# Kernel optimization log

Measured on AMD Instinct MI355X. Metric: run time of the kernel, lower is better.

## Reference

```python
import jax, jax.numpy as jnp
import numpy as np

N_NODES = 20000
T_STEPS = 8


def _layer_norm(x, g, b, eps=1e-5):
    mu = x.mean(-1, keepdims=True)
    var = ((x - mu) ** 2).mean(-1, keepdims=True)
    return (x - mu) * jax.lax.rsqrt(var + eps) * g + b


def _linear(x, W, b):
    # torch nn.Linear: x @ W.T + b, W is [out, in]
    return x @ W.T + b


def _gcn_conv(xw, norm, src, dst, b, n):
    # xw: pre-transformed features [N, H]; symmetric-normalized aggregation
    msg = xw[src] * norm[:, None]
    return jax.ops.segment_sum(msg, dst, num_segments=n) + b


def setup_inputs() -> dict:
    key = jax.random.key(0)
    ks = jax.random.split(key, 16)
    N, T, K, E, D, H, M = N_NODES, T_STEPS, 4000, 400000, 128, 128, 16
    s = 0.05
    return {
        "node_t": jax.random.randint(ks[0], (T, K), 0, N),
        "edge_index_t": jax.random.randint(ks[1], (T, 2, E), 0, N),
        "m": M,
        "emb": jax.random.normal(ks[2], (N, D), jnp.float32) * s,
        "convW1": jax.random.normal(ks[3], (H, D), jnp.float32) * s,
        "convb1": jnp.zeros((H,), jnp.float32),
        "convW2": jax.random.normal(ks[4], (H, H), jnp.float32) * s,
        "convb2": jnp.zeros((H,), jnp.float32),
        "tn_g": jnp.ones((H,), jnp.float32),
        "tn_b": jnp.zeros((H,), jnp.float32),
        "tok_w1": jax.random.normal(ks[5], (M, M), jnp.float32) * s,
        "tok_b1": jnp.zeros((M,), jnp.float32),
        "tok_w2": jax.random.normal(ks[6], (M, M), jnp.float32) * s,
        "tok_b2": jnp.zeros((M,), jnp.float32),
        "cn_g": jnp.ones((H,), jnp.float32),
        "cn_b": jnp.zeros((H,), jnp.float32),
        "ch_w1": jax.random.normal(ks[7], (H, H), jnp.float32) * s,
        "ch_b1": jnp.zeros((H,), jnp.float32),
        "ch_w2": jax.random.normal(ks[8], (H, H), jnp.float32) * s,
        "ch_b2": jnp.zeros((H,), jnp.float32),
    }


def reference(node_t, edge_index_t, m, emb, convW1, convb1, convW2, convb2,
              tn_g, tn_b, tok_w1, tok_b1, tok_w2, tok_b2,
              cn_g, cn_b, ch_w1, ch_b1, ch_w2, ch_b2):
    N = emb.shape[0]
    H = convW1.shape[0]
    gelu = lambda x: jax.nn.gelu(x, approximate=False)

    def mixer(x):  # x: [N, m, H]
        y = _layer_norm(x, tn_g, tn_b)
        y = jnp.swapaxes(y, 1, 2)                 # [N, H, m]
        y = _linear(gelu(_linear(y, tok_w1, tok_b1)), tok_w2, tok_b2)
        x = x + jnp.swapaxes(y, 1, 2)
        z = _layer_norm(x, cn_g, cn_b)
        z = _linear(gelu(_linear(z, ch_w1, ch_b1)), ch_w2, ch_b2)
        return x + z

    # conv linear transforms are per-node dense and constant w.r.t. step input emb
    xw1 = emb @ convW1.T                          # [N, H]
    self_loop = jnp.arange(N)

    def step(x_m, xs):
        node_i, edge_i = xs                        # [K], [2, E]
        x_m_new = mixer(x_m)
        x_new = x_m_new.mean(axis=1)               # FinalProcessLayer, discrete
        # GCN with self-loops and symmetric normalization
        src = jnp.concatenate([edge_i[0], self_loop])
        dst = jnp.concatenate([edge_i[1], self_loop])
        deg = jax.ops.segment_sum(jnp.ones_like(src, jnp.float32), dst,
                                  num_segments=N)
        dinv = jax.lax.rsqrt(jnp.maximum(deg, 1.0))
        norm = dinv[src] * dinv[dst]
        h = _gcn_conv(xw1, norm, src, dst, convb1, N)
        h = jax.nn.relu(h)
        h = _gcn_conv(h @ convW2.T, norm, src, dst, convb2, N)
        # zero rows of nodes present at this timestep (boolean-mask scatter)
        h = h.at[node_i].set(0.0)
        # slide window
        x_m = jnp.concatenate([x_m[:, 1:, :], h[:, None, :]], axis=1)
        return x_m, x_new

    x_m0 = jnp.zeros((N, m, H), jnp.float32)
    _, outs = jax.lax.scan(step, x_m0, (node_t, edge_index_t))
    return outs  # [T, N, H]
```

## Files before the change

kernel.cpp:

```cpp
#include <hip/hip_runtime.h>
#include <hip/hip_bf16.h>
#include <cstdint>
#include <cstddef>

#define NN 20000
#define HH 128
#define MM 16
#define KK 4000
#define EE 400000

typedef __attribute__((ext_vector_type(16))) float f16v;
typedef __attribute__((ext_vector_type(8))) short short8;
typedef __attribute__((ext_vector_type(4))) float f32x4;
typedef __attribute__((ext_vector_type(8), may_alias)) short s8ma;
typedef __attribute__((ext_vector_type(4), may_alias)) float f4ma;

__device__ __forceinline__ float gelu_f(float x) {
  return 0.5f * x * (1.0f + erff(x * 0.70710678118654752440f));
}

__device__ __forceinline__ unsigned short f2bf(float f) {
  union { float f; unsigned u; } v; v.f = f;
  unsigned u = v.u;
  unsigned r = (u + 0x7FFFu + ((u >> 16) & 1u)) >> 16;
  return (unsigned short)r;
}
__device__ __forceinline__ float bf2f(unsigned short s) {
  union { unsigned u; float f; } v; v.u = ((unsigned)s) << 16; return v.f;
}


__global__ void zero1_kernel(int* __restrict__ a, int n) {
  int i = blockIdx.x * 256 + threadIdx.x;
  if (i < n) a[i] = 0;
}

__global__ void count7_kernel(const int* __restrict__ edges, int* __restrict__ cnt7, int n7) {
  int e = blockIdx.x * 256 + threadIdx.x;
  if (e < n7) {
    int t = e / EE, i = e - t * EE;
    int d = edges[(size_t)t * 2 * EE + EE + i];
    atomicAdd(&cnt7[t * NN + d], 1);
  }
}

__global__ void dinv_kernel(const int* __restrict__ cnt, float* __restrict__ dinv, int n) {
  int i = blockIdx.x * 256 + threadIdx.x;
  if (i < n) dinv[i] = rsqrtf((float)(cnt[i] + 1));
}

__global__ void scan7_kernel(const int* __restrict__ cnt7, int* __restrict__ offs7) {
  __shared__ int sh[1024];
  __shared__ int carry_s;
  const int b = blockIdx.x;
  const int* cnt = cnt7 + b * NN;
  int* offs = offs7 + b * (NN + 1);
  int tid = threadIdx.x;
  if (tid == 0) carry_s = 0;
  __syncthreads();
  for (int base = 0; base < NN; base += 1024) {
    int i = base + tid;
    int v = (i < NN) ? cnt[i] : 0;
    sh[tid] = v;
    __syncthreads();
    for (int off = 1; off < 1024; off <<= 1) {
      int t = (tid >= off) ? sh[tid - off] : 0;
      __syncthreads();
      sh[tid] += t;
      __syncthreads();
    }
    int carry = carry_s;
    if (i < NN) offs[i] = carry + sh[tid] - v;
    __syncthreads();
    if (tid == 1023) carry_s = carry + sh[1023];
    __syncthreads();
  }
  if (tid == 0) offs[NN] = carry_s;
}

__global__ void fillcsr_kernel(const int* __restrict__ esrc, const int* __restrict__ edst,
                               const int* __restrict__ offs, int* __restrict__ cursor,
                               const float* __restrict__ dinv,
                               int* __restrict__ csrc, float* __restrict__ cnorm, int n) {
  int e = blockIdx.x * 256 + threadIdx.x;
  if (e < n) {
    int s = esrc[e], d = edst[e];
    int pos = offs[d] + atomicAdd(&cursor[d], 1);
    csrc[pos] = s;
    cnorm[pos] = dinv[s] * dinv[d];
  }
}

__global__ __launch_bounds__(128) void agg_kernel(const float* __restrict__ X,
    const int* __restrict__ csrc, const float* __restrict__ cnorm,
    const int* __restrict__ offs, const float* __restrict__ dinv,
    const float* __restrict__ bias, int relu, float* __restrict__ Y) {
  int i = blockIdx.x, c = threadIdx.x;
  float di = dinv[i];
  float acc = X[(size_t)i * HH + c] * di * di;
  int s = offs[i], e = offs[i + 1];
  for (int j = s; j < e; ++j) {
    acc += X[(size_t)csrc[j] * HH + c] * cnorm[j];
  }
  acc += bias[c];
  if (relu) acc = fmaxf(acc, 0.f);
  Y[(size_t)i * HH + c] = acc;
}

__global__ __launch_bounds__(128) void gemm128_kernel(const float* __restrict__ X,
    const float* __restrict__ W, float* __restrict__ Y, int nrows) {
  __shared__ float Ws[128 * 129];
  __shared__ float Xs[8 * 128];
  int tid = threadIdx.x;
  for (int idx = tid; idx < 16384; idx += 128) {
    int o = idx >> 7, k = idx & 127;
    Ws[o * 129 + k] = W[idx];
  }
  __syncthreads();
  for (int row0 = blockIdx.x * 8; row0 < nrows; row0 += gridDim.x * 8) {
    int nr = min(8, nrows - row0);
    for (int idx = tid; idx < nr * 128; idx += 128) Xs[idx] = X[(size_t)row0 * 128 + idx];
    __syncthreads();
    float acc[8] = {0, 0, 0, 0, 0, 0, 0, 0};
    for (int k = 0; k < 128; ++k) {
      float w = Ws[tid * 129 + k];
#pragma unroll
      for (int r = 0; r < 8; ++r) acc[r] += w * Xs[r * 128 + k];
    }
    for (int r = 0; r < nr; ++r) Y[(size_t)(row0 + r) * 128 + tid] = acc[r];
    __syncthreads();
  }
}

__global__ void mask_kernel(const int* __restrict__ nodes, float* __restrict__ H, int kn) {
  int idx = blockIdx.x * 256 + threadIdx.x;
  if (idx < kn * HH) {
    int j = idx >> 7, c = idx & 127;
    H[(size_t)nodes[j] * HH + c] = 0.f;
  }
}

__global__ void bcast_kernel(float* __restrict__ out, int total) {
  int idx = blockIdx.x * 256 + threadIdx.x + 128;
  if (idx < total) out[idx] = out[idx & 127];
}


__global__ __launch_bounds__(256) void mixer16_kernel(
    const float* __restrict__ hbufs,
    const float* __restrict__ tn_g, const float* __restrict__ tn_b,
    const float* __restrict__ tok_w1, const float* __restrict__ tok_b1,
    const float* __restrict__ tok_w2, const float* __restrict__ tok_b2,
    const float* __restrict__ cn_g, const float* __restrict__ cn_b,
    const float* __restrict__ ch_w1, const float* __restrict__ ch_b1,
    const float* __restrict__ ch_w2, const float* __restrict__ ch_b2,
    float* __restrict__ out, int total_items, int niter) {
  __shared__ __align__(16) float zw[64 * 132];
  __shared__ __align__(16) unsigned short zh[64 * 136];
  __shared__ __align__(16) unsigned short zl[64 * 136];
  __shared__ float fout[4 * 128];
  __shared__ float tg[128], tbv[128], cg[128], cbv[128], cb1v[128], cb2v[128];
  __shared__ float tw1s[256], tw2s[256], tb1s[16], tb2s[16];

  const int tid = threadIdx.x;
  const int lane = tid & 63;
  const int wv = tid >> 6;
  const int q = lane >> 4;
  const int h = lane & 15;

  if (tid < 128) {
    tg[tid] = tn_g[tid]; tbv[tid] = tn_b[tid];
    cg[tid] = cn_g[tid]; cbv[tid] = cn_b[tid];
    cb1v[tid] = ch_b1[tid]; cb2v[tid] = ch_b2[tid];
  }
  tw1s[tid] = tok_w1[tid];
  tw2s[tid] = tok_w2[tid];
  if (tid < 16) { tb1s[tid] = tok_b1[tid]; tb2s[tid] = tok_b2[tid]; }

  short8 wf1[4][2], wf2[4][2];
#pragma unroll
  for (int ks = 0; ks < 4; ++ks) {
#pragma unroll
    for (int j = 0; j < 2; ++j) {
      int o = (2 * wv + j) * 16 + h;
      int k0 = ks * 32 + q * 8;
      const float* s1 = ch_w1 + o * 128 + k0;
      const float* s2 = ch_w2 + o * 128 + k0;
      short8 p1, p2;
#pragma unroll
      for (int e = 0; e < 8; ++e) { p1[e] = (short)f2bf(s1[e]); p2[e] = (short)f2bf(s2[e]); }
      wf1[ks][j] = p1;
      wf2[ks][j] = p2;
    }
  }
  __syncthreads();

  const int lr = tid >> 2;
  const int lq = tid & 3;
  const int c2 = tid & 127;
  const int n0 = tid >> 7;

  for (int it = 0; it < niter; ++it) {
    const int item4 = it * gridDim.x + blockIdx.x;

    {
      const int n = lr >> 4, tok = lr & 15;
      const int item = item4 * 4 + n;
      const bool act = item < total_items;
      int t = 0, node = 0;
      if (act && item < 7 * NN) { t = item / NN + 1; node = item % NN; }
      int src_t = tok - (MM - t);
      f4ma x[8];
      if (act && src_t >= 0) {
        const float* hp = hbufs + ((size_t)src_t * NN + node) * HH + lq * 32;
#pragma unroll
        for (int j = 0; j < 8; ++j) x[j] = *(const f4ma*)(hp + 4 * j);
      } else {
#pragma unroll
        for (int j = 0; j < 8; ++j) x[j] = (f4ma){0.f, 0.f, 0.f, 0.f};
      }
      float s = 0.f, ss = 0.f;
#pragma unroll
      for (int j = 0; j < 8; ++j) {
        s += x[j].x + x[j].y + x[j].z + x[j].w;
        ss += x[j].x * x[j].x + x[j].y * x[j].y + x[j].z * x[j].z + x[j].w * x[j].w;
      }
      s += __shfl_xor(s, 1); ss += __shfl_xor(ss, 1);
      s += __shfl_xor(s, 2); ss += __shfl_xor(ss, 2);
      float mu = s * (1.f / 128.f);
      float var = fmaxf(ss * (1.f / 128.f) - mu * mu, 0.f);
      float rs = rsqrtf(var + 1e-5f);
#pragma unroll
      for (int j = 0; j < 8; ++j) *(f4ma*)&zw[lr * 132 + lq * 32 + 4 * j] = x[j];
      if (lq == 0) { zw[lr * 132 + 128] = mu; zw[lr * 132 + 129] = rs; }
    }
    __syncthreads();

    {
      const int rb0 = n0 * 16 * 132, rb1 = (n0 + 2) * 16 * 132;
      const float tgc = tg[c2], tbc = tbv[c2];
      f16v a0v, a1v;
#pragma unroll
      for (int hd = 0; hd < 16; ++hd) { float b = tb1s[hd]; a0v[hd] = b; a1v[hd] = b; }
#pragma unroll
      for (int r = 0; r < 16; ++r) {
        float x0 = zw[rb0 + r * 132 + c2];
        float m0 = zw[rb0 + r * 132 + 128], q0 = zw[rb0 + r * 132 + 129];
        float x1 = zw[rb1 + r * 132 + c2];
        float m1 = zw[rb1 + r * 132 + 128], q1 = zw[rb1 + r * 132 + 129];
        float z0 = (x0 - m0) * q0 * tgc + tbc;
        float z1 = (x1 - m1) * q1 * tgc + tbc;
#pragma unroll
        for (int hd = 0; hd < 16; ++hd) {
          float w = tw1s[hd * 16 + r];
          a0v[hd] += w * z0; a1v[hd] += w * z1;
        }
      }
#pragma unroll
      for (int hd = 0; hd < 16; ++hd) { a0v[hd] = gelu_f(a0v[hd]); a1v[hd] = gelu_f(a1v[hd]); }
      float cs0 = 0.f, cs1 = 0.f;
#pragma unroll
      for (int r = 0; r < 16; ++r) {
        float o0 = tb2s[r], o1 = tb2s[r];
#pragma unroll
        for (int hd = 0; hd < 16; ++hd) {
          float w = tw2s[r * 16 + hd];
          o0 += w * a0v[hd]; o1 += w * a1v[hd];
        }
        float nx0 = zw[rb0 + r * 132 + c2] + o0;
        float nx1 = zw[rb1 + r * 132 + c2] + o1;
        cs0 += nx0; cs1 += nx1;
        zw[rb0 + r * 132 + c2] = nx0;
        zw[rb1 + r * 132 + c2] = nx1;
      }
      fout[n0 * 128 + c2] = cs0;
      fout[(n0 + 2) * 128 + c2] = cs1;
    }
    __syncthreads();

    {
      f4ma x[8];
#pragma unroll
      for (int j = 0; j < 8; ++j) x[j] = *(const f4ma*)&zw[lr * 132 + lq * 32 + 4 * j];
      float s = 0.f, ss = 0.f;
#pragma unroll
      for (int j = 0; j < 8; ++j) {
        s += x[j].x + x[j].y + x[j].z + x[j].w;
        ss += x[j].x * x[j].x + x[j].y * x[j].y + x[j].z * x[j].z + x[j].w * x[j].w;
      }
      s += __shfl_xor(s, 1); ss += __shfl_xor(ss, 1);
      s += __shfl_xor(s, 2); ss += __shfl_xor(ss, 2);
      float mu = s * (1.f / 128.f);
      float var = fmaxf(ss * (1.f / 128.f) - mu * mu, 0.f);
      float rs = rsqrtf(var + 1e-5f);
#pragma unroll
      for (int j = 0; j < 4; ++j) {
        int c0 = lq * 32 + 8 * j;
        short8 ph, pl;
#pragma unroll
        for (int e = 0; e < 8; ++e) {
          int c = c0 + e;
          float xe = (e < 4) ? ((const float*)&x[2 * j])[e] : ((const float*)&x[2 * j + 1])[e - 4];
          float zf = (xe - mu) * rs * cg[c] + cbv[c];
          unsigned short hi = f2bf(zf);
          ph[e] = (short)hi;
          pl[e] = (short)f2bf(zf - bf2f(hi));
        }
        *(s8ma*)&zh[lr * 136 + c0] = (s8ma)ph;
        *(s8ma*)&zl[lr * 136 + c0] = (s8ma)pl;
      }
    }
    __syncthreads();

    {
      f32x4 acc[4][2];
#pragma unroll
      for (int rt = 0; rt < 4; ++rt) {
#pragma unroll
        for (int j = 0; j < 2; ++j) {
          float b = cb1v[(2 * wv + j) * 16 + h];
          acc[rt][j] = (f32x4){b, b, b, b};
        }
      }
#pragma unroll
      for (int ks = 0; ks < 4; ++ks) {
        const int col = ks * 32 + q * 8;
#pragma unroll
        for (int rt = 0; rt < 4; ++rt) {
          short8 ah = (short8)(*(const s8ma*)&zh[(rt * 16 + h) * 136 + col]);
          short8 al = (short8)(*(const s8ma*)&zl[(rt * 16 + h) * 136 + col]);
#pragma unroll
          for (int j = 0; j < 2; ++j) {
            acc[rt][j] = __builtin_amdgcn_mfma_f32_16x16x32_bf16(ah, wf1[ks][j], acc[rt][j], 0, 0, 0);
            acc[rt][j] = __builtin_amdgcn_mfma_f32_16x16x32_bf16(al, wf1[ks][j], acc[rt][j], 0, 0, 0);
          }
        }
      }
      __syncthreads();
#pragma unroll
      for (int rt = 0; rt < 4; ++rt) {
#pragma unroll
        for (int j = 0; j < 2; ++j) {
          int col = (2 * wv + j) * 16 + h;
#pragma unroll
          for (int rg = 0; rg < 4; ++rg) {
            int row = rt * 16 + q * 4 + rg;
            float v = gelu_f(acc[rt][j][rg]);
            unsigned short hi = f2bf(v);
            zh[row * 136 + col] = hi;
            zl[row * 136 + col] = f2bf(v - bf2f(hi));
          }
        }
      }
    }
    __syncthreads();

    {
      f32x4 acc[4][2];
#pragma unroll
      for (int rt = 0; rt < 4; ++rt) {
#pragma unroll
        for (int j = 0; j < 2; ++j) {
          float b = cb2v[(2 * wv + j) * 16 + h];
          acc[rt][j] = (f32x4){b, b, b, b};
        }
      }
#pragma unroll
      for (int ks = 0; ks < 4; ++ks) {
        const int col = ks * 32 + q * 8;
#pragma unroll
        for (int rt = 0; rt < 4; ++rt) {
          short8 ah = (short8)(*(const s8ma*)&zh[(rt * 16 + h) * 136 + col]);
          short8 al = (short8)(*(const s8ma*)&zl[(rt * 16 + h) * 136 + col]);
#pragma unroll
          for (int j = 0; j < 2; ++j) {
            acc[rt][j] = __builtin_amdgcn_mfma_f32_16x16x32_bf16(ah, wf2[ks][j], acc[rt][j], 0, 0, 0);
            acc[rt][j] = __builtin_amdgcn_mfma_f32_16x16x32_bf16(al, wf2[ks][j], acc[rt][j], 0, 0, 0);
          }
        }
      }
#pragma unroll
      for (int rt = 0; rt < 4; ++rt) {
        const int item = item4 * 4 + rt;
        const bool act = item < total_items;
        int t = 0, node = 0;
        if (act && item < 7 * NN) { t = item / NN + 1; node = item % NN; }
#pragma unroll
        for (int j = 0; j < 2; ++j) {
          float v = acc[rt][j][0] + acc[rt][j][1] + acc[rt][j][2] + acc[rt][j][3];
          v += __shfl_xor(v, 16);
          v += __shfl_xor(v, 32);
          if (q == 0 && act) {
            int col = (2 * wv + j) * 16 + h;
            out[((size_t)t * NN + node) * HH + col] = (fout[rt * 128 + col] + v) * (1.f / 16.f);
          }
        }
      }
    }
    __syncthreads();
  }
}


extern "C" void kernel_launch(void* const* d_in, const int* in_sizes, int n_in,
                              void* d_out, int out_size, void* d_ws, size_t ws_size,
                              hipStream_t stream) {
  const int* node_t   = (const int*)d_in[0];
  const int* edges    = (const int*)d_in[1];
  const float* emb    = (const float*)d_in[3];
  const float* convW1 = (const float*)d_in[4];
  const float* convb1 = (const float*)d_in[5];
  const float* convW2 = (const float*)d_in[6];
  const float* convb2 = (const float*)d_in[7];
  const float* tn_g   = (const float*)d_in[8];
  const float* tn_b   = (const float*)d_in[9];
  const float* tok_w1 = (const float*)d_in[10];
  const float* tok_b1 = (const float*)d_in[11];
  const float* tok_w2 = (const float*)d_in[12];
  const float* tok_b2 = (const float*)d_in[13];
  const float* cn_g   = (const float*)d_in[14];
  const float* cn_b   = (const float*)d_in[15];
  const float* ch_w1  = (const float*)d_in[16];
  const float* ch_b1  = (const float*)d_in[17];
  const float* ch_w2  = (const float*)d_in[18];
  const float* ch_b2  = (const float*)d_in[19];
  float* out = (float*)d_out;

  char* ws = (char*)d_ws;
  size_t off = 0;
  auto alloc = [&](size_t bytes) -> void* {
    void* p = ws + off;
    off += (bytes + 511) & ~(size_t)511;
    return p;
  };
  float* xw1   = (float*)alloc((size_t)NN * HH * 4);
  float* hbufs = (float*)alloc((size_t)7 * NN * HH * 4);
  float* h     = (float*)alloc((size_t)NN * HH * 4);
  float* h2    = (float*)alloc((size_t)NN * HH * 4);
  int*   cnt7  = (int*)alloc((size_t)7 * NN * 4);
  float* dinv7 = (float*)alloc((size_t)7 * NN * 4);
  int*   offs7 = (int*)alloc((size_t)7 * (NN + 1) * 4);
  int*   cursor= (int*)alloc((size_t)NN * 4);
  int*   csrc  = (int*)alloc((size_t)EE * 4);
  float* cnorm = (float*)alloc((size_t)EE * 4);

  gemm128_kernel<<<512, 128, 0, stream>>>(emb, convW1, xw1, NN);

  zero1_kernel<<<(7 * NN + 255) / 256, 256, 0, stream>>>(cnt7, 7 * NN);
  count7_kernel<<<(7 * EE + 255) / 256, 256, 0, stream>>>(edges, cnt7, 7 * EE);
  dinv_kernel<<<(7 * NN + 255) / 256, 256, 0, stream>>>(cnt7, dinv7, 7 * NN);
  scan7_kernel<<<7, 1024, 0, stream>>>(cnt7, offs7);

  for (int t = 0; t < 7; ++t) {
    const int* es = edges + (size_t)t * 2 * EE;
    const int* ed = es + EE;
    const int* offs = offs7 + (size_t)t * (NN + 1);
    const float* dinv = dinv7 + (size_t)t * NN;
    zero1_kernel<<<(NN + 255) / 256, 256, 0, stream>>>(cursor, NN);
    fillcsr_kernel<<<(EE + 255) / 256, 256, 0, stream>>>(es, ed, offs, cursor, dinv,
                                                         csrc, cnorm, EE);
    agg_kernel<<<NN, 128, 0, stream>>>(xw1, csrc, cnorm, offs, dinv, convb1, 1, h);
    gemm128_kernel<<<512, 128, 0, stream>>>(h, convW2, h2, NN);
    agg_kernel<<<NN, 128, 0, stream>>>(h2, csrc, cnorm, offs, dinv, convb2, 0,
                                       hbufs + (size_t)t * NN * HH);
    mask_kernel<<<(KK * HH + 255) / 256, 256, 0, stream>>>(
        node_t + (size_t)t * KK, hbufs + (size_t)t * NN * HH, KK);
  }

  const int total_items = 7 * NN + 1;
  const int nblocks = 2048;
  const int item4s = (total_items + 3) / 4;
  const int niter = (item4s + nblocks - 1) / nblocks;
  mixer16_kernel<<<nblocks, 256, 0, stream>>>(hbufs, tn_g, tn_b, tok_w1, tok_b1, tok_w2,
                                              tok_b2, cn_g, cn_b, ch_w1, ch_b1, ch_w2,
                                              ch_b2, out, total_items, niter);
  bcast_kernel<<<((NN * HH - 128) + 255) / 256, 256, 0, stream>>>(out, NN * HH);
}
```

Baseline: 3.365 ms.

## Double mixer block size to 8 items with 512 threads and one column tile per wave

The mixer kernel now handles 8 nodes (128 token rows) per block with 512 threads and 8 waves. Each wave owns a single 16-column output slice across 8 row tiles, instead of two slices across 4 row tiles. This halves the per-wave weight fragments held in registers and spreads the work over more waves per block. In exchange the block's shared-memory footprint roughly doubles, which may reduce how many blocks fit per CU.

```diff
diff --git a/kernel.cpp b/kernel.cpp
--- a/kernel.cpp
+++ b/kernel.cpp
@@ -146,7 +146,7 @@
 }
 
 
-__global__ __launch_bounds__(256) void mixer16_kernel(
+__global__ __launch_bounds__(512) void mixer17_kernel(
     const float* __restrict__ hbufs,
     const float* __restrict__ tn_g, const float* __restrict__ tn_b,
     const float* __restrict__ tok_w1, const float* __restrict__ tok_b1,
@@ -155,10 +155,10 @@
     const float* __restrict__ ch_w1, const float* __restrict__ ch_b1,
     const float* __restrict__ ch_w2, const float* __restrict__ ch_b2,
     float* __restrict__ out, int total_items, int niter) {
-  __shared__ __align__(16) float zw[64 * 132];
-  __shared__ __align__(16) unsigned short zh[64 * 136];
-  __shared__ __align__(16) unsigned short zl[64 * 136];
-  __shared__ float fout[4 * 128];
+  __shared__ __align__(16) float zw[128 * 132];
+  __shared__ __align__(16) unsigned short zh[128 * 136];
+  __shared__ __align__(16) unsigned short zl[128 * 136];
+  __shared__ float fout[8 * 128];
   __shared__ float tg[128], tbv[128], cg[128], cbv[128], cb1v[128], cb2v[128];
   __shared__ float tw1s[256], tw2s[256], tb1s[16], tb2s[16];
 
@@ -173,25 +173,21 @@
     cg[tid] = cn_g[tid]; cbv[tid] = cn_b[tid];
     cb1v[tid] = ch_b1[tid]; cb2v[tid] = ch_b2[tid];
   }
-  tw1s[tid] = tok_w1[tid];
-  tw2s[tid] = tok_w2[tid];
+  if (tid < 256) { tw1s[tid] = tok_w1[tid]; tw2s[tid] = tok_w2[tid]; }
   if (tid < 16) { tb1s[tid] = tok_b1[tid]; tb2s[tid] = tok_b2[tid]; }
 
-  short8 wf1[4][2], wf2[4][2];
+  short8 wf1[4], wf2[4];
 #pragma unroll
   for (int ks = 0; ks < 4; ++ks) {
-#pragma unroll
-    for (int j = 0; j < 2; ++j) {
-      int o = (2 * wv + j) * 16 + h;
-      int k0 = ks * 32 + q * 8;
-      const float* s1 = ch_w1 + o * 128 + k0;
-      const float* s2 = ch_w2 + o * 128 + k0;
-      short8 p1, p2;
-#pragma unroll
-      for (int e = 0; e < 8; ++e) { p1[e] = (short)f2bf(s1[e]); p2[e] = (short)f2bf(s2[e]); }
-      wf1[ks][j] = p1;
-      wf2[ks][j] = p2;
-    }
+    int o = wv * 16 + h;
+    int k0 = ks * 32 + q * 8;
+    const float* s1 = ch_w1 + o * 128 + k0;
+    const float* s2 = ch_w2 + o * 128 + k0;
+    short8 p1, p2;
+#pragma unroll
+    for (int e = 0; e < 8; ++e) { p1[e] = (short)f2bf(s1[e]); p2[e] = (short)f2bf(s2[e]); }
+    wf1[ks] = p1;
+    wf2[ks] = p2;
   }
   __syncthreads();
 
@@ -201,11 +197,11 @@
   const int n0 = tid >> 7;
 
   for (int it = 0; it < niter; ++it) {
-    const int item4 = it * gridDim.x + blockIdx.x;
+    const int item8 = it * gridDim.x + blockIdx.x;
 
     {
       const int n = lr >> 4, tok = lr & 15;
-      const int item = item4 * 4 + n;
+      const int item = item8 * 8 + n;
       const bool act = item < total_items;
       int t = 0, node = 0;
       if (act && item < 7 * NN) { t = item / NN + 1; node = item % NN; }
@@ -237,7 +233,7 @@
     __syncthreads();
 
     {
-      const int rb0 = n0 * 16 * 132, rb1 = (n0 + 2) * 16 * 132;
+      const int rb0 = n0 * 16 * 132, rb1 = (n0 + 4) * 16 * 132;
       const float tgc = tg[c2], tbc = tbv[c2];
       f16v a0v, a1v;
 #pragma unroll
@@ -274,7 +270,7 @@
         zw[rb1 + r * 132 + c2] = nx1;
       }
       fout[n0 * 128 + c2] = cs0;
-      fout[(n0 + 2) * 128 + c2] = cs1;
+      fout[(n0 + 4) * 128 + c2] = cs1;
     }
     __syncthreads();
 
@@ -313,87 +309,69 @@
     __syncthreads();
 
     {
-      f32x4 acc[4][2];
-#pragma unroll
-      for (int rt = 0; rt < 4; ++rt) {
-#pragma unroll
-        for (int j = 0; j < 2; ++j) {
-          float b = cb1v[(2 * wv + j) * 16 + h];
-          acc[rt][j] = (f32x4){b, b, b, b};
-        }
+      f32x4 acc[8];
+      {
+        float b = cb1v[wv * 16 + h];
+#pragma unroll
+        for (int rt = 0; rt < 8; ++rt) acc[rt] = (f32x4){b, b, b, b};
       }
 #pragma unroll
       for (int ks = 0; ks < 4; ++ks) {
         const int col = ks * 32 + q * 8;
 #pragma unroll
-        for (int rt = 0; rt < 4; ++rt) {
+        for (int rt = 0; rt < 8; ++rt) {
           short8 ah = (short8)(*(const s8ma*)&zh[(rt * 16 + h) * 136 + col]);
           short8 al = (short8)(*(const s8ma*)&zl[(rt * 16 + h) * 136 + col]);
-#pragma unroll
-          for (int j = 0; j < 2; ++j) {
-            acc[rt][j] = __builtin_amdgcn_mfma_f32_16x16x32_bf16(ah, wf1[ks][j], acc[rt][j], 0, 0, 0);
-            acc[rt][j] = __builtin_amdgcn_mfma_f32_16x16x32_bf16(al, wf1[ks][j], acc[rt][j], 0, 0, 0);
-          }
+          acc[rt] = __builtin_amdgcn_mfma_f32_16x16x32_bf16(ah, wf1[ks], acc[rt], 0, 0, 0);
+          acc[rt] = __builtin_amdgcn_mfma_f32_16x16x32_bf16(al, wf1[ks], acc[rt], 0, 0, 0);
         }
       }
       __syncthreads();
-#pragma unroll
-      for (int rt = 0; rt < 4; ++rt) {
-#pragma unroll
-        for (int j = 0; j < 2; ++j) {
-          int col = (2 * wv + j) * 16 + h;
-#pragma unroll
-          for (int rg = 0; rg < 4; ++rg) {
-            int row = rt * 16 + q * 4 + rg;
-            float v = gelu_f(acc[rt][j][rg]);
-            unsigned short hi = f2bf(v);
-            zh[row * 136 + col] = hi;
-            zl[row * 136 + col] = f2bf(v - bf2f(hi));
-          }
+      const int col = wv * 16 + h;
+#pragma unroll
+      for (int rt = 0; rt < 8; ++rt) {
+#pragma unroll
+        for (int rg = 0; rg < 4; ++rg) {
+          int row = rt * 16 + q * 4 + rg;
+          float v = gelu_f(acc[rt][rg]);
+          unsigned short hi = f2bf(v);
+          zh[row * 136 + col] = hi;
+          zl[row * 136 + col] = f2bf(v - bf2f(hi));
         }
       }
     }
     __syncthreads();
 
     {
-      f32x4 acc[4][2];
-#pragma unroll
-      for (int rt = 0; rt < 4; ++rt) {
-#pragma unroll
-        for (int j = 0; j < 2; ++j) {
-          float b = cb2v[(2 * wv + j) * 16 + h];
-          acc[rt][j] = (f32x4){b, b, b, b};
-        }
+      f32x4 acc[8];
+      {
+        float b = cb2v[wv * 16 + h];
+#pragma unroll
+        for (int rt = 0; rt < 8; ++rt) acc[rt] = (f32x4){b, b, b, b};
       }
 #pragma unroll
       for (int ks = 0; ks < 4; ++ks) {
         const int col = ks * 32 + q * 8;
 #pragma unroll
-        for (int rt = 0; rt < 4; ++rt) {
+        for (int rt = 0; rt < 8; ++rt) {
           short8 ah = (short8)(*(const s8ma*)&zh[(rt * 16 + h) * 136 + col]);
           short8 al = (short8)(*(const s8ma*)&zl[(rt * 16 + h) * 136 + col]);
-#pragma unroll
-          for (int j = 0; j < 2; ++j) {
-            acc[rt][j] = __builtin_amdgcn_mfma_f32_16x16x32_bf16(ah, wf2[ks][j], acc[rt][j], 0, 0, 0);
-            acc[rt][j] = __builtin_amdgcn_mfma_f32_16x16x32_bf16(al, wf2[ks][j], acc[rt][j], 0, 0, 0);
-          }
-        }
-      }
-#pragma unroll
-      for (int rt = 0; rt < 4; ++rt) {
-        const int item = item4 * 4 + rt;
+          acc[rt] = __builtin_amdgcn_mfma_f32_16x16x32_bf16(ah, wf2[ks], acc[rt], 0, 0, 0);
+          acc[rt] = __builtin_amdgcn_mfma_f32_16x16x32_bf16(al, wf2[ks], acc[rt], 0, 0, 0);
+        }
+      }
+      const int col = wv * 16 + h;
+#pragma unroll
+      for (int rt = 0; rt < 8; ++rt) {
+        const int item = item8 * 8 + rt;
         const bool act = item < total_items;
         int t = 0, node = 0;
         if (act && item < 7 * NN) { t = item / NN + 1; node = item % NN; }
-#pragma unroll
-        for (int j = 0; j < 2; ++j) {
-          float v = acc[rt][j][0] + acc[rt][j][1] + acc[rt][j][2] + acc[rt][j][3];
-          v += __shfl_xor(v, 16);
-          v += __shfl_xor(v, 32);
-          if (q == 0 && act) {
-            int col = (2 * wv + j) * 16 + h;
-            out[((size_t)t * NN + node) * HH + col] = (fout[rt * 128 + col] + v) * (1.f / 16.f);
-          }
+        float v = acc[rt][0] + acc[rt][1] + acc[rt][2] + acc[rt][3];
+        v += __shfl_xor(v, 16);
+        v += __shfl_xor(v, 32);
+        if (q == 0 && act) {
+          out[((size_t)t * NN + node) * HH + col] = (fout[rt * 128 + col] + v) * (1.f / 16.f);
         }
       }
     }
@@ -468,10 +446,10 @@
   }
 
   const int total_items = 7 * NN + 1;
-  const int nblocks = 2048;
-  const int item4s = (total_items + 3) / 4;
-  const int niter = (item4s + nblocks - 1) / nblocks;
-  mixer16_kernel<<<nblocks, 256, 0, stream>>>(hbufs, tn_g, tn_b, tok_w1, tok_b1, tok_w2,
+  const int nblocks = 1024;
+  const int item8s = (total_items + 7) / 8;
+  const int niter = (item8s + nblocks - 1) / nblocks;
+  mixer17_kernel<<<nblocks, 512, 0, stream>>>(hbufs, tn_g, tn_b, tok_w1, tok_b1, tok_w2,
                                               tok_b2, cn_g, cn_b, ch_w1, ch_b1, ch_w2,
                                               ch_b2, out, total_items, niter);
   bcast_kernel<<<((NN * HH - 128) + 255) / 256, 256, 0, stream>>>(out, NN * HH);
```

After: 4.886 ms. +45.2%, slower.

## Batch all seven GCN timesteps into single launches when workspace allows

Applied to the files above, without the earlier changes.

Replaces the per-timestep loop of CSR fill, two aggregations, GEMM and mask with single kernels covering all seven timesteps, indexed by a time offset, when the workspace holds at least 260 MB. The goal is to cut the per-step launch overhead and the small, under-filled grids (40 kernels down to about 6) and to expose more parallelism per launch. The cost is extra workspace for per-step CSR arrays and intermediate feature buffers, and the old looped path is kept as a fallback.

```diff
diff --git a/kernel.cpp b/kernel.cpp
--- a/kernel.cpp
+++ b/kernel.cpp
@@ -78,33 +78,42 @@
   if (tid == 0) offs[NN] = carry_s;
 }
 
-__global__ void fillcsr_kernel(const int* __restrict__ esrc, const int* __restrict__ edst,
-                               const int* __restrict__ offs, int* __restrict__ cursor,
-                               const float* __restrict__ dinv,
-                               int* __restrict__ csrc, float* __restrict__ cnorm, int n) {
+__global__ void fillcsr7_kernel(const int* __restrict__ edges,
+                                const int* __restrict__ offs7, int* __restrict__ cursor7,
+                                const float* __restrict__ dinv7,
+                                int* __restrict__ csrc7, float* __restrict__ cnorm7, int n7) {
   int e = blockIdx.x * 256 + threadIdx.x;
-  if (e < n) {
-    int s = esrc[e], d = edst[e];
-    int pos = offs[d] + atomicAdd(&cursor[d], 1);
-    csrc[pos] = s;
-    cnorm[pos] = dinv[s] * dinv[d];
-  }
-}
-
-__global__ __launch_bounds__(128) void agg_kernel(const float* __restrict__ X,
-    const int* __restrict__ csrc, const float* __restrict__ cnorm,
-    const int* __restrict__ offs, const float* __restrict__ dinv,
-    const float* __restrict__ bias, int relu, float* __restrict__ Y) {
-  int i = blockIdx.x, c = threadIdx.x;
+  if (e < n7) {
+    int t = e / EE, i = e - t * EE;
+    const int* es = edges + (size_t)t * 2 * EE;
+    int s = es[i], d = es[EE + i];
+    int pos = offs7[t * (NN + 1) + d] + atomicAdd(&cursor7[t * NN + d], 1);
+    csrc7[(size_t)t * EE + pos] = s;
+    cnorm7[(size_t)t * EE + pos] = dinv7[t * NN + s] * dinv7[t * NN + d];
+  }
+}
+
+__global__ __launch_bounds__(128) void agg7_kernel(const float* __restrict__ X,
+    const int* __restrict__ csrc7, const float* __restrict__ cnorm7,
+    const int* __restrict__ offs7, const float* __restrict__ dinv7,
+    const float* __restrict__ bias, int relu, float* __restrict__ Y, int xshared) {
+  const int b = blockIdx.x;
+  const int t = b / NN, i = b - t * NN;
+  const int c = threadIdx.x;
+  const int* csrc = csrc7 + (size_t)t * EE;
+  const float* cnorm = cnorm7 + (size_t)t * EE;
+  const int* offs = offs7 + t * (NN + 1);
+  const float* dinv = dinv7 + t * NN;
+  const float* Xt = xshared ? X : X + (size_t)t * NN * HH;
   float di = dinv[i];
-  float acc = X[(size_t)i * HH + c] * di * di;
-  int s = offs[i], e = offs[i + 1];
-  for (int j = s; j < e; ++j) {
-    acc += X[(size_t)csrc[j] * HH + c] * cnorm[j];
+  float acc = Xt[(size_t)i * HH + c] * di * di;
+  int s0 = offs[i], e0 = offs[i + 1];
+  for (int j = s0; j < e0; ++j) {
+    acc += Xt[(size_t)csrc[j] * HH + c] * cnorm[j];
   }
   acc += bias[c];
   if (relu) acc = fmaxf(acc, 0.f);
-  Y[(size_t)i * HH + c] = acc;
+  Y[(size_t)b * HH + c] = acc;
 }
 
 __global__ __launch_bounds__(128) void gemm128_kernel(const float* __restrict__ X,
@@ -132,11 +141,12 @@
   }
 }
 
-__global__ void mask_kernel(const int* __restrict__ nodes, float* __restrict__ H, int kn) {
+__global__ void mask7_kernel(const int* __restrict__ node_t, float* __restrict__ hb, int n) {
   int idx = blockIdx.x * 256 + threadIdx.x;
-  if (idx < kn * HH) {
-    int j = idx >> 7, c = idx & 127;
-    H[(size_t)nodes[j] * HH + c] = 0.f;
+  if (idx < n) {
+    int t = idx / (KK * HH), r = idx - t * KK * HH;
+    int j = r >> 7, c = r & 127;
+    hb[((size_t)t * NN + node_t[t * KK + j]) * HH + c] = 0.f;
   }
 }
 
@@ -435,14 +445,12 @@
   };
   float* xw1   = (float*)alloc((size_t)NN * HH * 4);
   float* hbufs = (float*)alloc((size_t)7 * NN * HH * 4);
-  float* h     = (float*)alloc((size_t)NN * HH * 4);
-  float* h2    = (float*)alloc((size_t)NN * HH * 4);
   int*   cnt7  = (int*)alloc((size_t)7 * NN * 4);
   float* dinv7 = (float*)alloc((size_t)7 * NN * 4);
   int*   offs7 = (int*)alloc((size_t)7 * (NN + 1) * 4);
-  int*   cursor= (int*)alloc((size_t)NN * 4);
-  int*   csrc  = (int*)alloc((size_t)EE * 4);
-  float* cnorm = (float*)alloc((size_t)EE * 4);
+  int*   cursor7 = (int*)alloc((size_t)7 * NN * 4);
+
+  const bool batched = ws_size >= (size_t)260 * 1024 * 1024;
 
   gemm128_kernel<<<512, 128, 0, stream>>>(emb, convW1, xw1, NN);
 
@@ -451,20 +459,40 @@
   dinv_kernel<<<(7 * NN + 255) / 256, 256, 0, stream>>>(cnt7, dinv7, 7 * NN);
   scan7_kernel<<<7, 1024, 0, stream>>>(cnt7, offs7);
 
-  for (int t = 0; t < 7; ++t) {
-    const int* es = edges + (size_t)t * 2 * EE;
-    const int* ed = es + EE;
-    const int* offs = offs7 + (size_t)t * (NN + 1);
-    const float* dinv = dinv7 + (size_t)t * NN;
-    zero1_kernel<<<(NN + 255) / 256, 256, 0, stream>>>(cursor, NN);
-    fillcsr_kernel<<<(EE + 255) / 256, 256, 0, stream>>>(es, ed, offs, cursor, dinv,
-                                                         csrc, cnorm, EE);
-    agg_kernel<<<NN, 128, 0, stream>>>(xw1, csrc, cnorm, offs, dinv, convb1, 1, h);
-    gemm128_kernel<<<512, 128, 0, stream>>>(h, convW2, h2, NN);
-    agg_kernel<<<NN, 128, 0, stream>>>(h2, csrc, cnorm, offs, dinv, convb2, 0,
-                                       hbufs + (size_t)t * NN * HH);
-    mask_kernel<<<(KK * HH + 255) / 256, 256, 0, stream>>>(
-        node_t + (size_t)t * KK, hbufs + (size_t)t * NN * HH, KK);
+  if (batched) {
+    int*   csrc7  = (int*)alloc((size_t)7 * EE * 4);
+    float* cnorm7 = (float*)alloc((size_t)7 * EE * 4);
+    float* h7     = (float*)alloc((size_t)7 * NN * HH * 4);
+    float* g7     = (float*)alloc((size_t)7 * NN * HH * 4);
+
+    zero1_kernel<<<(7 * NN + 255) / 256, 256, 0, stream>>>(cursor7, 7 * NN);
+    fillcsr7_kernel<<<(7 * EE + 255) / 256, 256, 0, stream>>>(edges, offs7, cursor7,
+                                                              dinv7, csrc7, cnorm7, 7 * EE);
+    agg7_kernel<<<7 * NN, 128, 0, stream>>>(xw1, csrc7, cnorm7, offs7, dinv7,
+                                            convb1, 1, h7, 1);
+    gemm128_kernel<<<2048, 128, 0, stream>>>(h7, convW2, g7, 7 * NN);
+    agg7_kernel<<<7 * NN, 128, 0, stream>>>(g7, csrc7, cnorm7, offs7, dinv7,
+                                            convb2, 0, hbufs, 0);
+    mask7_kernel<<<(7 * KK * HH + 255) / 256, 256, 0, stream>>>(node_t, hbufs, 7 * KK * HH);
+  } else {
+    int*   csrc  = (int*)alloc((size_t)EE * 4);
+    float* cnorm = (float*)alloc((size_t)EE * 4);
+    float* h1    = (float*)alloc((size_t)NN * HH * 4);
+    float* g1    = (float*)alloc((size_t)NN * HH * 4);
+    for (int t = 0; t < 7; ++t) {
+      const int* offs = offs7 + (size_t)t * (NN + 1);
+      const float* dinv = dinv7 + (size_t)t * NN;
+      zero1_kernel<<<(NN + 255) / 256, 256, 0, stream>>>(cursor7, NN);
+      fillcsr7_kernel<<<(EE + 255) / 256, 256, 0, stream>>>(edges + (size_t)t * 2 * EE,
+                                                            offs, cursor7, dinv, csrc, cnorm, EE);
+      agg7_kernel<<<NN, 128, 0, stream>>>(xw1, csrc, cnorm, offs, dinv, convb1, 1, h1, 1);
+      gemm128_kernel<<<512, 128, 0, stream>>>(h1, convW2, g1, NN);
+      agg7_kernel<<<NN, 128, 0, stream>>>(g1, csrc, cnorm, offs, dinv, convb2, 0,
+                                          hbufs + (size_t)t * NN * HH, 0);
+      mask7_kernel<<<(KK * HH + 255) / 256, 256, 0, stream>>>(node_t + (size_t)t * KK,
+                                                              hbufs + (size_t)t * NN * HH,
+                                                              KK * HH);
+    }
   }
 
   const int total_items = 7 * NN + 1;
```

New measurement: 3.229 ms. 1.04x faster.
